# Optimization experiments

Hardware: AMD Instinct MI355X
Metric: run time of the kernel (lower is better)

## Reference

```python
import jax, jax.numpy as jnp
import numpy as np

NEG_MASK = -999.0  # matches masked_fill_(-999) in the torch source

def setup_inputs() -> dict:
    key = jax.random.key(0)
    ks = jax.random.split(key, 8)
    B, N, D = 4, 2048, 768      # batch, nodes, in_dim
    H, Do = 6, 128              # att_head, out_dim (D == H*Do)
    feat_in = jax.random.normal(ks[0], (B, N, D), dtype=jnp.float32)
    adj = jax.random.randint(ks[1], (B, N, N), 0, 2).astype(jnp.int32)
    W = jax.random.normal(ks[2], (H, D, Do), dtype=jnp.float32) * (1.0 / np.sqrt(D))
    b = jnp.zeros((Do,), dtype=jnp.float32)
    w_src = jax.random.normal(ks[3], (H, Do, 1), dtype=jnp.float32) * (1.0 / np.sqrt(Do))
    w_dst = jax.random.normal(ks[4], (H, Do, 1), dtype=jnp.float32) * (1.0 / np.sqrt(Do))
    H_w = jax.random.normal(ks[5], (D, D), dtype=jnp.float32) * (1.0 / np.sqrt(D))
    H_b = jnp.zeros((D,), dtype=jnp.float32)
    return {"feat_in": feat_in, "adj": adj, "W": W, "b": b,
            "w_src": w_src, "w_dst": w_dst, "H_w": H_w, "H_b": H_b}

def reference(feat_in, adj, W, b, w_src, w_dst, H_w, H_b):
    leaky_alpha = 0.2
    B, N, D = feat_in.shape
    Hh = W.shape[0]
    # per-head projection: [B, H, N, Do]
    h = jnp.einsum('bni,hio->bhno', feat_in, W)
    th = jnp.tanh(h)
    attn_src = jnp.einsum('bhno,hoz->bhnz', th, w_src)  # [B,H,N,1]
    attn_dst = jnp.einsum('bhno,hoz->bhnz', th, w_dst)  # [B,H,N,1]
    # additive scores: src_i + dst_j -> [B,H,N,N]
    attn = attn_src + jnp.swapaxes(attn_dst, -1, -2)
    attn = jnp.where(attn >= 0, attn, leaky_alpha * attn)
    mask = (adj == 0)[:, None, :, :]  # [B,1,N,N]
    attn = jnp.where(mask, NEG_MASK, attn)
    attn = jax.nn.softmax(attn, axis=-1)
    feat_out = jnp.einsum('bhnm,bhmo->bhno', attn, h) + b  # [B,H,N,Do]
    feat_out = jnp.swapaxes(feat_out, 1, 2).reshape(B, N, -1)  # [B,N,H*Do]
    feat_out = jax.nn.elu(feat_out)
    gate = jax.nn.sigmoid(feat_in @ H_w.T + H_b)
    out = gate * feat_out + (1.0 - gate) * feat_in
    return out
```

## Files before the change

### kernel.cpp

```cpp
#include <hip/hip_runtime.h>
#include <hip/hip_bf16.h>

#define B_ 4
#define N_ 2048
#define D_ 768
#define H_ 6
#define Do_ 128
#define M_ (B_*N_)
#define C2_ (2*D_)
#define SROW 49152

typedef __attribute__((ext_vector_type(8))) short bf16x8;
typedef __attribute__((ext_vector_type(4))) float f32x4;
typedef __attribute__((ext_vector_type(4))) int int4v;
typedef __attribute__((ext_vector_type(2))) int int2v;
typedef __attribute__((ext_vector_type(4))) float float4v;
typedef __attribute__((ext_vector_type(4))) unsigned short ushort4v;

__device__ __forceinline__ float b2f(short s){
    unsigned u = ((unsigned)(unsigned short)s) << 16;
    return __builtin_bit_cast(float, u);
}
__device__ __forceinline__ short f2b(float f){
    unsigned u = __builtin_bit_cast(unsigned, f);
    unsigned r = (u + 0x7fffu + ((u >> 16) & 1u)) >> 16;
    return (short)r;
}
__device__ __forceinline__ int pk2(float a, float b){
    unsigned ua = __builtin_bit_cast(unsigned, a) + 0x8000u;
    unsigned ub = __builtin_bit_cast(unsigned, b) + 0x8000u;
    return (int)__builtin_amdgcn_perm(ub, ua, 0x07060302u);
}
__device__ __forceinline__ float fast_tanh(float x){
    float a = fabsf(x);
    float e = __expf(-2.0f * a);
    float t = (1.0f - e) / (1.0f + e);
    return copysignf(t, x);
}

__global__ __launch_bounds__(256) void k_prep_pack(const float* __restrict__ W,
                                                   const float* __restrict__ Hw,
                                                   const int* __restrict__ adj,
                                                   short* __restrict__ bmat,
                                                   unsigned char* __restrict__ pk){
    int bid = blockIdx.x, t = threadIdx.x;
    if (bid < C2_){
        int c = bid;
        if (c < D_){
            int hd = c >> 7, o = c & 127;
            const float* wp = W + hd*D_*Do_ + o;
            for (int k = t; k < D_; k += 256) bmat[c*D_ + k] = f2b(wp[k*Do_]);
        } else {
            int d = c - D_;
            const float* hp = Hw + d*D_;
            for (int k = t; k < D_; k += 256) bmat[c*D_ + k] = f2b(hp[k]);
        }
    } else {
        int g = (bid - C2_)*256 + t;
        const int* ap = adj + (size_t)g*8;
        int4v a0 = *(const int4v*)ap;
        int4v a1 = *(const int4v*)(ap + 4);
        unsigned by = 0;
        #pragma unroll
        for (int i = 0; i < 4; i++){
            by |= (a0[i] ? 1u : 0u) << i;
            by |= (a1[i] ? 1u : 0u) << (i + 4);
        }
        pk[g] = (unsigned char)by;
    }
}

__global__ __launch_bounds__(256) void k_gemm(const float* __restrict__ A,
                                              const short* __restrict__ Bm,
                                              short* __restrict__ ht,
                                              float* outg){
    __shared__ short As[128][72];
    __shared__ short Bs[128][72];
    int tid = threadIdx.x;
    int mBase = blockIdx.y * 128, cBase = blockIdx.x * 128;
    int wave = tid >> 6, lane = tid & 63, q = lane >> 4, nL = lane & 15;
    int wr = (wave >> 1) * 64, wc = (wave & 1) * 64;
    f32x4 acc[4][4] = {};
    for (int kk = 0; kk < D_; kk += 64){
        __syncthreads();
        #pragma unroll
        for (int i = 0; i < 8; i++){
            int idx = tid + i*256;
            int row = idx >> 4, c4 = (idx & 15) * 4;
            float4v av = *(const float4v*)&A[(mBase+row)*D_ + kk + c4];
            int2v w; w[0] = pk2(av[0], av[1]); w[1] = pk2(av[2], av[3]);
            *(int2v*)&As[row][c4] = w;
        }
        #pragma unroll
        for (int i = 0; i < 4; i++){
            int idx = tid + i*256;
            int row = idx >> 3, cs = (idx & 7) * 8;
            *(int4v*)&Bs[row][cs] = *(const int4v*)&Bm[(cBase+row)*D_ + kk + cs];
        }
        __syncthreads();
        #pragma unroll
        for (int k2 = 0; k2 < 64; k2 += 32){
            bf16x8 aF[4], bF[4];
            #pragma unroll
            for (int rt = 0; rt < 4; rt++) aF[rt] = *(const bf16x8*)&As[wr + rt*16 + nL][k2 + q*8];
            #pragma unroll
            for (int ct = 0; ct < 4; ct++) bF[ct] = *(const bf16x8*)&Bs[wc + ct*16 + nL][k2 + q*8];
            #pragma unroll
            for (int rt = 0; rt < 4; rt++)
                #pragma unroll
                for (int ct = 0; ct < 4; ct++)
                    acc[rt][ct] = __builtin_amdgcn_mfma_f32_16x16x32_bf16(aF[rt], bF[ct], acc[rt][ct], 0, 0, 0);
        }
    }
    if (cBase < D_){
        int hd = cBase >> 7;
        #pragma unroll
        for (int rt = 0; rt < 4; rt++){
            #pragma unroll
            for (int ct = 0; ct < 4; ct++){
                int o  = (wc + ct*16 + nL) & 127;
                int m0 = mBase + wr + rt*16 + q*4;
                int b = m0 >> 11, n0 = m0 & 2047;
                ushort4v v;
                #pragma unroll
                for (int r = 0; r < 4; r++) v[r] = (unsigned short)f2b(acc[rt][ct][r]);
                *(ushort4v*)&ht[((b*H_ + hd)*Do_ + o)*N_ + n0] = v;
            }
        }
    } else {
        #pragma unroll
        for (int rt = 0; rt < 4; rt++){
            #pragma unroll
            for (int ct = 0; ct < 4; ct++){
                int d  = cBase - D_ + wc + ct*16 + nL;
                int m0 = mBase + wr + rt*16 + q*4;
                #pragma unroll
                for (int r = 0; r < 4; r++) outg[(size_t)(m0 + r)*D_ + d] = acc[rt][ct][r];
            }
        }
    }
}

__global__ __launch_bounds__(256) void k_stats(const short* __restrict__ ht,
                                               const float* __restrict__ wsrc,
                                               const float* __restrict__ wdst,
                                               float* __restrict__ srcP,
                                               float* __restrict__ dstP){
    int g = blockIdx.x * 256 + threadIdx.x;
    int y = blockIdx.y, o0 = y * 32;
    int bh = g >> 11, n = g & 2047;
    int hd = bh % H_;
    const short* hp = ht + bh*Do_*N_ + n + o0*N_;
    const float* ws = wsrc + hd*Do_ + o0;
    const float* wd = wdst + hd*Do_ + o0;
    float as = 0.f, ad = 0.f;
    for (int o = 0; o < 32; o++){
        float t = fast_tanh(b2f(hp[o*N_]));
        as += t * ws[o];
        ad += t * wd[o];
    }
    srcP[y*SROW + g] = as; dstP[y*SROW + g] = ad;
}

struct StageS {
    float E1[2048];
    float E2[2048];
    unsigned pkw[64*65];
};
struct RedS { float red[2][64][37]; };
union LdsU { StageS s; RedS r; };
__global__ __launch_bounds__(256) void k_pv(const unsigned char* __restrict__ pkG,
                                            const float* __restrict__ srcP,
                                            const float* __restrict__ dstP,
                                            const short* __restrict__ ht,
                                            const float* __restrict__ feat_in,
                                            const float* __restrict__ bias,
                                            const float* __restrict__ Hb,
                                            float* outg){
    __shared__ LdsU U;
    int itile = blockIdx.x, hd = blockIdx.y, b = blockIdx.z;
    int tid = threadIdx.x, wave = tid >> 6, lane = tid & 63, q = lane >> 4, nL = lane & 15;
    int rh = wave >> 1, kh = wave & 1;
    int r0 = itile * 64;
    int bh = b*H_ + hd;
    {
        const float4v* g0 = (const float4v*)(dstP + bh*N_);
        const float4v* g1 = (const float4v*)(dstP + SROW + bh*N_);
        const float4v* g2 = (const float4v*)(dstP + 2*SROW + bh*N_);
        const float4v* g3 = (const float4v*)(dstP + 3*SROW + bh*N_);
        #pragma unroll
        for (int h = 0; h < 2; h++){
            int c4 = tid*2 + h;
            float4v d = g0[c4] + g1[c4] + g2[c4] + g3[c4];
            #pragma unroll
            for (int t = 0; t < 4; t++){
                U.s.E1[c4*4 + t] = __expf(d[t]);
                U.s.E2[c4*4 + t] = __expf(0.2f * d[t]);
            }
        }
        const unsigned* pg = (const unsigned*)(pkG + (size_t)(b*N_ + r0) * (N_/8));
        #pragma unroll
        for (int k = 0; k < 16; k++){
            int idx = tid + k*256;
            U.s.pkw[(idx >> 6)*65 + (idx & 63)] = pg[idx];
        }
    }
    __syncthreads();
    int rowL0 = rh*32 + nL, rowL1 = rowL0 + 16;
    int gi0 = bh*N_ + r0 + rowL0, gi1 = bh*N_ + r0 + rowL1;
    float s0 = srcP[gi0] + srcP[SROW+gi0] + srcP[2*SROW+gi0] + srcP[3*SROW+gi0];
    float s1 = srcP[gi1] + srcP[SROW+gi1] + srcP[2*SROW+gi1] + srcP[3*SROW+gi1];
    float e1r0 = __expf(s0), e2r0 = __expf(0.2f*s0);
    float e1r1 = __expf(s1), e2r1 = __expf(0.2f*s1);
    bf16x8 vone;
    #pragma unroll
    for (int t = 0; t < 8; t++) vone[t] = (short)0x3F80;
    const short* hp = ht + bh*Do_*N_;
    f32x4 acc[2][8] = {};
    f32x4 accl0 = {}, accl1 = {};
    int base0 = rowL0*65, base1 = rowL1*65;
    int jEnd = kh*1024 + 1024;
    for (int j0 = kh*1024; j0 < jEnd; j0 += 32){
        unsigned by0 = (U.s.pkw[base0 + (j0 >> 5)] >> (q*8)) & 0xFF;
        unsigned by1 = (U.s.pkw[base1 + (j0 >> 5)] >> (q*8)) & 0xFF;
        int kb = j0 + q*8;
        float4v E1a = *(const float4v*)&U.s.E1[kb];
        float4v E1b = *(const float4v*)&U.s.E1[kb + 4];
        float4v E2a = *(const float4v*)&U.s.E2[kb];
        float4v E2b = *(const float4v*)&U.s.E2[kb + 4];
        float p0[8], p1[8];
        #pragma unroll
        for (int t = 0; t < 8; t++){
            float E1t = t < 4 ? E1a[t] : E1b[t-4];
            float E2t = t < 4 ? E2a[t] : E2b[t-4];
            float a0 = fmaxf(e1r0*E1t, e2r0*E2t);
            float a1 = fmaxf(e1r1*E1t, e2r1*E2t);
            p0[t] = ((by0 >> t) & 1u) ? a0 : 0.0f;
            p1[t] = ((by1 >> t) & 1u) ? a1 : 0.0f;
        }
        int4v pi0, pi1;
        #pragma unroll
        for (int tp = 0; tp < 4; tp++){
            pi0[tp] = pk2(p0[2*tp], p0[2*tp+1]);
            pi1[tp] = pk2(p1[2*tp], p1[2*tp+1]);
        }
        bf16x8 pf0 = __builtin_bit_cast(bf16x8, pi0);
        bf16x8 pf1 = __builtin_bit_cast(bf16x8, pi1);
        #pragma unroll
        for (int ct = 0; ct < 8; ct++){
            bf16x8 bF = *(const bf16x8*)&hp[(ct*16 + nL)*N_ + kb];
            acc[0][ct] = __builtin_amdgcn_mfma_f32_16x16x32_bf16(pf0, bF, acc[0][ct], 0, 0, 0);
            acc[1][ct] = __builtin_amdgcn_mfma_f32_16x16x32_bf16(pf1, bF, acc[1][ct], 0, 0, 0);
        }
        accl0 = __builtin_amdgcn_mfma_f32_16x16x32_bf16(pf0, vone, accl0, 0, 0, 0);
        accl1 = __builtin_amdgcn_mfma_f32_16x16x32_bf16(pf1, vone, accl1, 0, 0, 0);
    }
    __syncthreads();
    if (kh == 1){
        #pragma unroll
        for (int ct = 0; ct < 8; ct++)
            #pragma unroll
            for (int r = 0; r < 4; r++) U.r.red[rh][lane][ct*4 + r] = acc[0][ct][r];
        #pragma unroll
        for (int r = 0; r < 4; r++) U.r.red[rh][lane][32 + r] = accl0[r];
    }
    __syncthreads();
    if (kh == 0){
        #pragma unroll
        for (int ct = 0; ct < 8; ct++)
            #pragma unroll
            for (int r = 0; r < 4; r++) acc[0][ct][r] += U.r.red[rh][lane][ct*4 + r];
        #pragma unroll
        for (int r = 0; r < 4; r++) accl0[r] += U.r.red[rh][lane][32 + r];
    }
    __syncthreads();
    if (kh == 0){
        #pragma unroll
        for (int ct = 0; ct < 8; ct++)
            #pragma unroll
            for (int r = 0; r < 4; r++) U.r.red[rh][lane][ct*4 + r] = acc[1][ct][r];
        #pragma unroll
        for (int r = 0; r < 4; r++) U.r.red[rh][lane][32 + r] = accl1[r];
    }
    __syncthreads();
    if (kh == 1){
        #pragma unroll
        for (int ct = 0; ct < 8; ct++)
            #pragma unroll
            for (int r = 0; r < 4; r++) acc[1][ct][r] += U.r.red[rh][lane][ct*4 + r];
        #pragma unroll
        for (int r = 0; r < 4; r++) accl1[r] += U.r.red[rh][lane][32 + r];
    }
    {
        int f = kh;
        f32x4 accl = f ? accl1 : accl0;
        #pragma unroll
        for (int r = 0; r < 4; r++){
            int i = r0 + rh*32 + f*16 + q*4 + r;
            float invl = 1.0f / accl[r];
            size_t base = (size_t)(b*N_ + i)*D_ + hd*Do_;
            #pragma unroll
            for (int ct = 0; ct < 8; ct++){
                int o = ct*16 + nL;
                float v = acc[f][ct][r]*invl + bias[o];
                float e = v > 0.f ? v : __expf(v) - 1.0f;
                float gl = outg[base + o] + Hb[hd*Do_ + o];
                float g = 1.0f / (1.0f + __expf(-gl));
                float fi = feat_in[base + o];
                outg[base + o] = g*e + (1.0f - g)*fi;
            }
        }
    }
}

extern "C" void kernel_launch(void* const* d_in, const int* in_sizes, int n_in,
                              void* d_out, int out_size, void* d_ws, size_t ws_size,
                              hipStream_t stream){
    const float* feat = (const float*)d_in[0];
    const int*   adj  = (const int*)  d_in[1];
    const float* W    = (const float*)d_in[2];
    const float* bias = (const float*)d_in[3];
    const float* wsrc = (const float*)d_in[4];
    const float* wdst = (const float*)d_in[5];
    const float* Hw   = (const float*)d_in[6];
    const float* Hb   = (const float*)d_in[7];
    float* out = (float*)d_out;
    char* ws = (char*)d_ws;
    short* bmat = (short*)(ws);
    short* ht   = (short*)(ws + 2359296);
    float* srcP = (float*)(ws + 14942208);
    float* dstP = (float*)(ws + 15728640);
    unsigned char* pk = (unsigned char*)(ws + 16515072);

    hipLaunchKernelGGL(k_prep_pack, dim3(C2_ + 8192), dim3(256), 0, stream, W, Hw, adj, bmat, pk);
    hipLaunchKernelGGL(k_gemm,      dim3(12, 64),     dim3(256), 0, stream, feat, bmat, ht, out);
    hipLaunchKernelGGL(k_stats,     dim3(192, 4),     dim3(256), 0, stream, ht, wsrc, wdst, srcP, dstP);
    hipLaunchKernelGGL(k_pv,        dim3(32, 6, 4),   dim3(256), 0, stream, pk, srcP, dstP,
                       ht, feat, bias, Hb, out);
}
```

Before: 317.6 us.

## Tile ht layout, async global-to-LDS loads, swizzled LDS, XCD-aware block remap

Changes the projected-feature buffer to a tiled [bh][n/32][o][32] layout so the attention PV kernel reads contiguous 64-byte chunks instead of rows strided by N. The GEMM now loads fp32 A and bf16 B directly into XOR-swizzled LDS via global_load_lds, converts to bf16 with the hardware pack instruction at fragment-load time, and stages the gate-output epilogue through LDS for coalesced float4 stores. Both GEMM and PV grids are flattened and remapped so consecutive blocks spread across the 8 XCDs. The PV inner loop uses packed float2 math, bit-field-extract masks and v_cvt_pk_bf16_f32 in place of a select-then-pack sequence. In exchange the A tile stays fp32 in LDS, doubling its footprint, and the cvt happens repeatedly per wave.

```diff
diff --git a/kernel.cpp b/kernel.cpp
--- a/kernel.cpp
+++ b/kernel.cpp
@@ -13,8 +13,8 @@
 typedef __attribute__((ext_vector_type(8))) short bf16x8;
 typedef __attribute__((ext_vector_type(4))) float f32x4;
 typedef __attribute__((ext_vector_type(4))) int int4v;
-typedef __attribute__((ext_vector_type(2))) int int2v;
 typedef __attribute__((ext_vector_type(4))) float float4v;
+typedef __attribute__((ext_vector_type(2))) float float2v;
 typedef __attribute__((ext_vector_type(4))) unsigned short ushort4v;
 
 __device__ __forceinline__ float b2f(short s){
@@ -26,10 +26,10 @@
     unsigned r = (u + 0x7fffu + ((u >> 16) & 1u)) >> 16;
     return (short)r;
 }
-__device__ __forceinline__ int pk2(float a, float b){
-    unsigned ua = __builtin_bit_cast(unsigned, a) + 0x8000u;
-    unsigned ub = __builtin_bit_cast(unsigned, b) + 0x8000u;
-    return (int)__builtin_amdgcn_perm(ub, ua, 0x07060302u);
+__device__ __forceinline__ int cvtpk(float lo, float hi){
+    int r;
+    asm("v_cvt_pk_bf16_f32 %0, %1, %2" : "=v"(r) : "v"(lo), "v"(hi));
+    return r;
 }
 __device__ __forceinline__ float fast_tanh(float x){
     float a = fabsf(x);
@@ -37,6 +37,13 @@
     float t = (1.0f - e) / (1.0f + e);
     return copysignf(t, x);
 }
+__device__ __forceinline__ void gload_lds16(const void* g, void* l){
+    __builtin_amdgcn_global_load_lds((const __attribute__((address_space(1))) unsigned int*)g,
+                                     (__attribute__((address_space(3))) unsigned int*)l,
+                                     16, 0, 0);
+}
+
+#define HT_IDX(bh, n, o) ((((size_t)((bh)*64 + ((n) >> 5))*128 + (o))*32) + ((n) & 31))
 
 __global__ __launch_bounds__(256) void k_prep_pack(const float* __restrict__ W,
                                                    const float* __restrict__ Hw,
@@ -70,41 +77,59 @@
     }
 }
 
-__global__ __launch_bounds__(256) void k_gemm(const float* __restrict__ A,
+union GS {
+    struct { float A[8192]; short B[8192]; } s;
+    float t[12288];
+};
+__global__ __launch_bounds__(256) void k_gemm(const float* __restrict__ Af,
                                               const short* __restrict__ Bm,
                                               short* __restrict__ ht,
                                               float* outg){
-    __shared__ short As[128][72];
-    __shared__ short Bs[128][72];
-    int tid = threadIdx.x;
-    int mBase = blockIdx.y * 128, cBase = blockIdx.x * 128;
-    int wave = tid >> 6, lane = tid & 63, q = lane >> 4, nL = lane & 15;
+    __shared__ GS G;
+    int lid = blockIdx.x;
+    int nid = (lid & 7)*96 + (lid >> 3);
+    int bx = nid % 12, by = nid / 12;
+    int mBase = by * 128, cBase = bx * 128;
+    int tid = threadIdx.x, wave = tid >> 6, lane = tid & 63, q = lane >> 4, nL = lane & 15;
     int wr = (wave >> 1) * 64, wc = (wave & 1) * 64;
+    int arow = tid >> 4;
+    int alu  = (tid & 15) ^ (arow & 7);
+    const float* aSrc = Af + (size_t)(mBase + arow)*D_ + alu*4;
+    float* aDst = G.t + wave*256;
+    int brow = tid >> 3;
+    int blu  = (tid & 7) ^ (brow & 7);
+    const short* bSrc = Bm + (size_t)(cBase + brow)*D_ + blu*8;
+    short* bDst = G.s.B + wave*512;
     f32x4 acc[4][4] = {};
     for (int kk = 0; kk < D_; kk += 64){
         __syncthreads();
         #pragma unroll
-        for (int i = 0; i < 8; i++){
-            int idx = tid + i*256;
-            int row = idx >> 4, c4 = (idx & 15) * 4;
-            float4v av = *(const float4v*)&A[(mBase+row)*D_ + kk + c4];
-            int2v w; w[0] = pk2(av[0], av[1]); w[1] = pk2(av[2], av[3]);
-            *(int2v*)&As[row][c4] = w;
-        }
-        #pragma unroll
-        for (int i = 0; i < 4; i++){
-            int idx = tid + i*256;
-            int row = idx >> 3, cs = (idx & 7) * 8;
-            *(int4v*)&Bs[row][cs] = *(const int4v*)&Bm[(cBase+row)*D_ + kk + cs];
-        }
+        for (int i = 0; i < 8; i++)
+            gload_lds16(aSrc + (size_t)i*16*D_ + kk, aDst + i*1024);
+        #pragma unroll
+        for (int i = 0; i < 4; i++)
+            gload_lds16(bSrc + (size_t)i*32*D_ + kk, bDst + i*2048);
         __syncthreads();
         #pragma unroll
         for (int k2 = 0; k2 < 64; k2 += 32){
+            int ub = (k2 >> 2) + q*2;
             bf16x8 aF[4], bF[4];
             #pragma unroll
-            for (int rt = 0; rt < 4; rt++) aF[rt] = *(const bf16x8*)&As[wr + rt*16 + nL][k2 + q*8];
-            #pragma unroll
-            for (int ct = 0; ct < 4; ct++) bF[ct] = *(const bf16x8*)&Bs[wc + ct*16 + nL][k2 + q*8];
+            for (int rt = 0; rt < 4; rt++){
+                int r = wr + rt*16 + nL;
+                const float* Ar = &G.s.A[r*64];
+                float4v x0 = *(const float4v*)&Ar[(ub ^ (r & 7)) << 2];
+                float4v x1 = *(const float4v*)&Ar[((ub+1) ^ (r & 7)) << 2];
+                int4v w = { cvtpk(x0[0], x0[1]), cvtpk(x0[2], x0[3]),
+                            cvtpk(x1[0], x1[1]), cvtpk(x1[2], x1[3]) };
+                aF[rt] = __builtin_bit_cast(bf16x8, w);
+            }
+            int cb = (k2 >> 3) + q;
+            #pragma unroll
+            for (int ct = 0; ct < 4; ct++){
+                int r = wc + ct*16 + nL;
+                bF[ct] = *(const bf16x8*)&G.s.B[r*64 + ((cb ^ (r & 7)) * 8)];
+            }
             #pragma unroll
             for (int rt = 0; rt < 4; rt++)
                 #pragma unroll
@@ -121,22 +146,33 @@
                 int o  = (wc + ct*16 + nL) & 127;
                 int m0 = mBase + wr + rt*16 + q*4;
                 int b = m0 >> 11, n0 = m0 & 2047;
+                int bh = b*H_ + hd;
                 ushort4v v;
                 #pragma unroll
                 for (int r = 0; r < 4; r++) v[r] = (unsigned short)f2b(acc[rt][ct][r]);
-                *(ushort4v*)&ht[((b*H_ + hd)*Do_ + o)*N_ + n0] = v;
+                *(ushort4v*)&ht[HT_IDX(bh, n0, o)] = v;
             }
         }
     } else {
+        __syncthreads();
+        int dQ = cBase - D_ + wc;
+        float* Ts = G.t + wave*1088;
+        int row = lane >> 2, cbs = (lane & 3) * 16;
         #pragma unroll
         for (int rt = 0; rt < 4; rt++){
             #pragma unroll
-            for (int ct = 0; ct < 4; ct++){
-                int d  = cBase - D_ + wc + ct*16 + nL;
-                int m0 = mBase + wr + rt*16 + q*4;
+            for (int ct = 0; ct < 4; ct++)
                 #pragma unroll
-                for (int r = 0; r < 4; r++) outg[(size_t)(m0 + r)*D_ + d] = acc[rt][ct][r];
-            }
+                for (int r = 0; r < 4; r++)
+                    Ts[(q*4 + r)*68 + ct*16 + nL] = acc[rt][ct][r];
+            __builtin_amdgcn_sched_barrier(0);
+            int gm = mBase + wr + rt*16 + row;
+            #pragma unroll
+            for (int c4 = 0; c4 < 4; c4++){
+                float4v v = *(const float4v*)&Ts[row*68 + cbs + c4*4];
+                *(float4v*)&outg[(size_t)gm*D_ + dQ + cbs + c4*4] = v;
+            }
+            __builtin_amdgcn_sched_barrier(0);
         }
     }
 }
@@ -150,12 +186,12 @@
     int y = blockIdx.y, o0 = y * 32;
     int bh = g >> 11, n = g & 2047;
     int hd = bh % H_;
-    const short* hp = ht + bh*Do_*N_ + n + o0*N_;
+    const short* hp = ht + HT_IDX(bh, n, o0);
     const float* ws = wsrc + hd*Do_ + o0;
     const float* wd = wdst + hd*Do_ + o0;
     float as = 0.f, ad = 0.f;
     for (int o = 0; o < 32; o++){
-        float t = fast_tanh(b2f(hp[o*N_]));
+        float t = fast_tanh(b2f(hp[o*32]));
         as += t * ws[o];
         ad += t * wd[o];
     }
@@ -178,7 +214,10 @@
                                             const float* __restrict__ Hb,
                                             float* outg){
     __shared__ LdsU U;
-    int itile = blockIdx.x, hd = blockIdx.y, b = blockIdx.z;
+    int lid = blockIdx.x;
+    int nid = (lid & 7)*96 + (lid >> 3);
+    int itile = nid & 31;
+    int hd = (nid >> 5) % 6, b = nid / 192;
     int tid = threadIdx.x, wave = tid >> 6, lane = tid & 63, q = lane >> 4, nL = lane & 15;
     int rh = wave >> 1, kh = wave & 1;
     int r0 = itile * 64;
@@ -210,12 +249,12 @@
     int gi0 = bh*N_ + r0 + rowL0, gi1 = bh*N_ + r0 + rowL1;
     float s0 = srcP[gi0] + srcP[SROW+gi0] + srcP[2*SROW+gi0] + srcP[3*SROW+gi0];
     float s1 = srcP[gi1] + srcP[SROW+gi1] + srcP[2*SROW+gi1] + srcP[3*SROW+gi1];
-    float e1r0 = __expf(s0), e2r0 = __expf(0.2f*s0);
-    float e1r1 = __expf(s1), e2r1 = __expf(0.2f*s1);
+    float2v e1v0 = {__expf(s0), __expf(s0)}, e2v0 = {__expf(0.2f*s0), __expf(0.2f*s0)};
+    float2v e1v1 = {__expf(s1), __expf(s1)}, e2v1 = {__expf(0.2f*s1), __expf(0.2f*s1)};
     bf16x8 vone;
     #pragma unroll
     for (int t = 0; t < 8; t++) vone[t] = (short)0x3F80;
-    const short* hp = ht + bh*Do_*N_;
+    const short* hp = ht + (size_t)bh*262144;
     f32x4 acc[2][8] = {};
     f32x4 accl0 = {}, accl1 = {};
     int base0 = rowL0*65, base1 = rowL1*65;
@@ -224,31 +263,29 @@
         unsigned by0 = (U.s.pkw[base0 + (j0 >> 5)] >> (q*8)) & 0xFF;
         unsigned by1 = (U.s.pkw[base1 + (j0 >> 5)] >> (q*8)) & 0xFF;
         int kb = j0 + q*8;
-        float4v E1a = *(const float4v*)&U.s.E1[kb];
-        float4v E1b = *(const float4v*)&U.s.E1[kb + 4];
-        float4v E2a = *(const float4v*)&U.s.E2[kb];
-        float4v E2b = *(const float4v*)&U.s.E2[kb + 4];
-        float p0[8], p1[8];
-        #pragma unroll
-        for (int t = 0; t < 8; t++){
-            float E1t = t < 4 ? E1a[t] : E1b[t-4];
-            float E2t = t < 4 ? E2a[t] : E2b[t-4];
-            float a0 = fmaxf(e1r0*E1t, e2r0*E2t);
-            float a1 = fmaxf(e1r1*E1t, e2r1*E2t);
-            p0[t] = ((by0 >> t) & 1u) ? a0 : 0.0f;
-            p1[t] = ((by1 >> t) & 1u) ? a1 : 0.0f;
-        }
-        int4v pi0, pi1;
+        const short* hj = hp + (size_t)(j0 >> 5)*4096 + q*8;
+        const float2v* E1p = (const float2v*)&U.s.E1[kb];
+        const float2v* E2p = (const float2v*)&U.s.E2[kb];
+        int w0[4], w1[4];
         #pragma unroll
         for (int tp = 0; tp < 4; tp++){
-            pi0[tp] = pk2(p0[2*tp], p0[2*tp+1]);
-            pi1[tp] = pk2(p1[2*tp], p1[2*tp+1]);
-        }
+            float2v E1t = E1p[tp], E2t = E2p[tp];
+            float2v a0 = __builtin_elementwise_max(e1v0*E1t, e2v0*E2t);
+            float2v a1 = __builtin_elementwise_max(e1v1*E1t, e2v1*E2t);
+            int m00 = __builtin_amdgcn_sbfe((int)by0, 2*tp,   1);
+            int m01 = __builtin_amdgcn_sbfe((int)by0, 2*tp+1, 1);
+            int m10 = __builtin_amdgcn_sbfe((int)by1, 2*tp,   1);
+            int m11 = __builtin_amdgcn_sbfe((int)by1, 2*tp+1, 1);
+            w0[tp] = cvtpk(a0[0], a0[1]) & (int)__builtin_amdgcn_perm((unsigned)m01, (unsigned)m00, 0x05040100u);
+            w1[tp] = cvtpk(a1[0], a1[1]) & (int)__builtin_amdgcn_perm((unsigned)m11, (unsigned)m10, 0x05040100u);
+        }
+        int4v pi0 = {w0[0], w0[1], w0[2], w0[3]};
+        int4v pi1 = {w1[0], w1[1], w1[2], w1[3]};
         bf16x8 pf0 = __builtin_bit_cast(bf16x8, pi0);
         bf16x8 pf1 = __builtin_bit_cast(bf16x8, pi1);
         #pragma unroll
         for (int ct = 0; ct < 8; ct++){
-            bf16x8 bF = *(const bf16x8*)&hp[(ct*16 + nL)*N_ + kb];
+            bf16x8 bF = *(const bf16x8*)&hj[(ct*16 + nL)*32];
             acc[0][ct] = __builtin_amdgcn_mfma_f32_16x16x32_bf16(pf0, bF, acc[0][ct], 0, 0, 0);
             acc[1][ct] = __builtin_amdgcn_mfma_f32_16x16x32_bf16(pf1, bF, acc[1][ct], 0, 0, 0);
         }
@@ -333,8 +370,8 @@
     unsigned char* pk = (unsigned char*)(ws + 16515072);
 
     hipLaunchKernelGGL(k_prep_pack, dim3(C2_ + 8192), dim3(256), 0, stream, W, Hw, adj, bmat, pk);
-    hipLaunchKernelGGL(k_gemm,      dim3(12, 64),     dim3(256), 0, stream, feat, bmat, ht, out);
+    hipLaunchKernelGGL(k_gemm,      dim3(768),        dim3(256), 0, stream, feat, bmat, ht, out);
     hipLaunchKernelGGL(k_stats,     dim3(192, 4),     dim3(256), 0, stream, ht, wsrc, wdst, srcP, dstP);
-    hipLaunchKernelGGL(k_pv,        dim3(32, 6, 4),   dim3(256), 0, stream, pk, srcP, dstP,
+    hipLaunchKernelGGL(k_pv,        dim3(768),        dim3(256), 0, stream, pk, srcP, dstP,
                        ht, feat, bias, Hb, out);
 }
```

New measurement: 287.1 us. 1.11x faster.

## Tile ht layout, remap grids for XCD locality, widen k_pv to 512 threads

Applied to the files above, without the earlier changes.

Changes the projected-feature buffer to a tiled layout (32-node chunks × 128 features), so the P·V B-fragment loads in k_pv and the strided loads in k_stats read contiguous 64-byte chunks instead of rows 4 KB apart. Remaps the GEMM and attention grids to 1D with an XCD-aware swizzle so blocks sharing data land on the same XCD and its L2. Stages the gate-GEMM output through LDS so it is written to global memory as coalesced float4 stores. k_pv now runs 8 waves, each handling 16 rows instead of 32, which raises parallelism but doubles the ht fragment loads per row tile and changes occupancy.

```diff
diff --git a/kernel.cpp b/kernel.cpp
--- a/kernel.cpp
+++ b/kernel.cpp
@@ -37,6 +37,8 @@
     float t = (1.0f - e) / (1.0f + e);
     return copysignf(t, x);
 }
+
+#define HT_IDX(bh, n, o) ((((size_t)((bh)*64 + ((n) >> 5))*128 + (o))*32) + ((n) & 31))
 
 __global__ __launch_bounds__(256) void k_prep_pack(const float* __restrict__ W,
                                                    const float* __restrict__ Hw,
@@ -76,8 +78,11 @@
                                               float* outg){
     __shared__ short As[128][72];
     __shared__ short Bs[128][72];
+    int lid = blockIdx.x;
+    int xcd = lid & 7, s = lid >> 3;
+    int bx = s >> 3, by = xcd*8 + (s & 7);
     int tid = threadIdx.x;
-    int mBase = blockIdx.y * 128, cBase = blockIdx.x * 128;
+    int mBase = by * 128, cBase = bx * 128;
     int wave = tid >> 6, lane = tid & 63, q = lane >> 4, nL = lane & 15;
     int wr = (wave >> 1) * 64, wc = (wave & 1) * 64;
     f32x4 acc[4][4] = {};
@@ -121,22 +126,33 @@
                 int o  = (wc + ct*16 + nL) & 127;
                 int m0 = mBase + wr + rt*16 + q*4;
                 int b = m0 >> 11, n0 = m0 & 2047;
+                int bh = b*H_ + hd;
                 ushort4v v;
                 #pragma unroll
                 for (int r = 0; r < 4; r++) v[r] = (unsigned short)f2b(acc[rt][ct][r]);
-                *(ushort4v*)&ht[((b*H_ + hd)*Do_ + o)*N_ + n0] = v;
+                *(ushort4v*)&ht[HT_IDX(bh, n0, o)] = v;
             }
         }
     } else {
+        __syncthreads();
+        int dQ = cBase - D_ + wc;
+        float* Ts = (float*)As + wave*1088;
+        int row = lane >> 2, cbs = (lane & 3) * 16;
         #pragma unroll
         for (int rt = 0; rt < 4; rt++){
             #pragma unroll
-            for (int ct = 0; ct < 4; ct++){
-                int d  = cBase - D_ + wc + ct*16 + nL;
-                int m0 = mBase + wr + rt*16 + q*4;
+            for (int ct = 0; ct < 4; ct++)
                 #pragma unroll
-                for (int r = 0; r < 4; r++) outg[(size_t)(m0 + r)*D_ + d] = acc[rt][ct][r];
+                for (int r = 0; r < 4; r++)
+                    Ts[(q*4 + r)*68 + ct*16 + nL] = acc[rt][ct][r];
+            __builtin_amdgcn_sched_barrier(0);
+            int gm = mBase + wr + rt*16 + row;
+            #pragma unroll
+            for (int c4 = 0; c4 < 4; c4++){
+                float4v v = *(const float4v*)&Ts[row*68 + cbs + c4*4];
+                *(float4v*)&outg[(size_t)gm*D_ + dQ + cbs + c4*4] = v;
             }
+            __builtin_amdgcn_sched_barrier(0);
         }
     }
 }
@@ -150,12 +166,12 @@
     int y = blockIdx.y, o0 = y * 32;
     int bh = g >> 11, n = g & 2047;
     int hd = bh % H_;
-    const short* hp = ht + bh*Do_*N_ + n + o0*N_;
+    const short* hp = ht + HT_IDX(bh, n, o0);
     const float* ws = wsrc + hd*Do_ + o0;
     const float* wd = wdst + hd*Do_ + o0;
     float as = 0.f, ad = 0.f;
     for (int o = 0; o < 32; o++){
-        float t = fast_tanh(b2f(hp[o*N_]));
+        float t = fast_tanh(b2f(hp[o*32]));
         as += t * ws[o];
         ad += t * wd[o];
     }
@@ -167,9 +183,9 @@
     float E2[2048];
     unsigned pkw[64*65];
 };
-struct RedS { float red[2][64][37]; };
+struct RedS { float red[4][64][37]; };
 union LdsU { StageS s; RedS r; };
-__global__ __launch_bounds__(256) void k_pv(const unsigned char* __restrict__ pkG,
+__global__ __launch_bounds__(512) void k_pv(const unsigned char* __restrict__ pkG,
                                             const float* __restrict__ srcP,
                                             const float* __restrict__ dstP,
                                             const short* __restrict__ ht,
@@ -178,7 +194,10 @@
                                             const float* __restrict__ Hb,
                                             float* outg){
     __shared__ LdsU U;
-    int itile = blockIdx.x, hd = blockIdx.y, b = blockIdx.z;
+    int lid = blockIdx.x;
+    int nid = (lid & 7)*96 + (lid >> 3);
+    int itile = nid & 31;
+    int hd = (nid >> 5) % 6, b = nid / 192;
     int tid = threadIdx.x, wave = tid >> 6, lane = tid & 63, q = lane >> 4, nL = lane & 15;
     int rh = wave >> 1, kh = wave & 1;
     int r0 = itile * 64;
@@ -188,126 +207,91 @@
         const float4v* g1 = (const float4v*)(dstP + SROW + bh*N_);
         const float4v* g2 = (const float4v*)(dstP + 2*SROW + bh*N_);
         const float4v* g3 = (const float4v*)(dstP + 3*SROW + bh*N_);
-        #pragma unroll
-        for (int h = 0; h < 2; h++){
-            int c4 = tid*2 + h;
-            float4v d = g0[c4] + g1[c4] + g2[c4] + g3[c4];
-            #pragma unroll
-            for (int t = 0; t < 4; t++){
-                U.s.E1[c4*4 + t] = __expf(d[t]);
-                U.s.E2[c4*4 + t] = __expf(0.2f * d[t]);
-            }
+        int c4 = tid;
+        float4v d = g0[c4] + g1[c4] + g2[c4] + g3[c4];
+        #pragma unroll
+        for (int t = 0; t < 4; t++){
+            U.s.E1[c4*4 + t] = __expf(d[t]);
+            U.s.E2[c4*4 + t] = __expf(0.2f * d[t]);
         }
         const unsigned* pg = (const unsigned*)(pkG + (size_t)(b*N_ + r0) * (N_/8));
         #pragma unroll
-        for (int k = 0; k < 16; k++){
-            int idx = tid + k*256;
+        for (int k = 0; k < 8; k++){
+            int idx = tid + k*512;
             U.s.pkw[(idx >> 6)*65 + (idx & 63)] = pg[idx];
         }
     }
     __syncthreads();
-    int rowL0 = rh*32 + nL, rowL1 = rowL0 + 16;
-    int gi0 = bh*N_ + r0 + rowL0, gi1 = bh*N_ + r0 + rowL1;
-    float s0 = srcP[gi0] + srcP[SROW+gi0] + srcP[2*SROW+gi0] + srcP[3*SROW+gi0];
-    float s1 = srcP[gi1] + srcP[SROW+gi1] + srcP[2*SROW+gi1] + srcP[3*SROW+gi1];
-    float e1r0 = __expf(s0), e2r0 = __expf(0.2f*s0);
-    float e1r1 = __expf(s1), e2r1 = __expf(0.2f*s1);
+    int rowL = rh*16 + nL;
+    int gi = bh*N_ + r0 + rowL;
+    float sv = srcP[gi] + srcP[SROW+gi] + srcP[2*SROW+gi] + srcP[3*SROW+gi];
+    float e1r = __expf(sv), e2r = __expf(0.2f*sv);
     bf16x8 vone;
     #pragma unroll
     for (int t = 0; t < 8; t++) vone[t] = (short)0x3F80;
-    const short* hp = ht + bh*Do_*N_;
-    f32x4 acc[2][8] = {};
-    f32x4 accl0 = {}, accl1 = {};
-    int base0 = rowL0*65, base1 = rowL1*65;
+    const short* hp = ht + (size_t)bh*262144;
+    f32x4 acc[8] = {};
+    f32x4 accl = {};
+    int base = rowL*65;
     int jEnd = kh*1024 + 1024;
     for (int j0 = kh*1024; j0 < jEnd; j0 += 32){
-        unsigned by0 = (U.s.pkw[base0 + (j0 >> 5)] >> (q*8)) & 0xFF;
-        unsigned by1 = (U.s.pkw[base1 + (j0 >> 5)] >> (q*8)) & 0xFF;
+        unsigned by = (U.s.pkw[base + (j0 >> 5)] >> (q*8)) & 0xFF;
         int kb = j0 + q*8;
+        const short* hj = hp + (size_t)(j0 >> 5)*4096 + q*8;
         float4v E1a = *(const float4v*)&U.s.E1[kb];
         float4v E1b = *(const float4v*)&U.s.E1[kb + 4];
         float4v E2a = *(const float4v*)&U.s.E2[kb];
         float4v E2b = *(const float4v*)&U.s.E2[kb + 4];
-        float p0[8], p1[8];
+        float p[8];
         #pragma unroll
         for (int t = 0; t < 8; t++){
             float E1t = t < 4 ? E1a[t] : E1b[t-4];
             float E2t = t < 4 ? E2a[t] : E2b[t-4];
-            float a0 = fmaxf(e1r0*E1t, e2r0*E2t);
-            float a1 = fmaxf(e1r1*E1t, e2r1*E2t);
-            p0[t] = ((by0 >> t) & 1u) ? a0 : 0.0f;
-            p1[t] = ((by1 >> t) & 1u) ? a1 : 0.0f;
-        }
-        int4v pi0, pi1;
-        #pragma unroll
-        for (int tp = 0; tp < 4; tp++){
-            pi0[tp] = pk2(p0[2*tp], p0[2*tp+1]);
-            pi1[tp] = pk2(p1[2*tp], p1[2*tp+1]);
-        }
-        bf16x8 pf0 = __builtin_bit_cast(bf16x8, pi0);
-        bf16x8 pf1 = __builtin_bit_cast(bf16x8, pi1);
+            float a = fmaxf(e1r*E1t, e2r*E2t);
+            p[t] = ((by >> t) & 1u) ? a : 0.0f;
+        }
+        int4v pi;
+        #pragma unroll
+        for (int tp = 0; tp < 4; tp++) pi[tp] = pk2(p[2*tp], p[2*tp+1]);
+        bf16x8 pf = __builtin_bit_cast(bf16x8, pi);
         #pragma unroll
         for (int ct = 0; ct < 8; ct++){
-            bf16x8 bF = *(const bf16x8*)&hp[(ct*16 + nL)*N_ + kb];
-            acc[0][ct] = __builtin_amdgcn_mfma_f32_16x16x32_bf16(pf0, bF, acc[0][ct], 0, 0, 0);
-            acc[1][ct] = __builtin_amdgcn_mfma_f32_16x16x32_bf16(pf1, bF, acc[1][ct], 0, 0, 0);
-        }
-        accl0 = __builtin_amdgcn_mfma_f32_16x16x32_bf16(pf0, vone, accl0, 0, 0, 0);
-        accl1 = __builtin_amdgcn_mfma_f32_16x16x32_bf16(pf1, vone, accl1, 0, 0, 0);
+            bf16x8 bF = *(const bf16x8*)&hj[(ct*16 + nL)*32];
+            acc[ct] = __builtin_amdgcn_mfma_f32_16x16x32_bf16(pf, bF, acc[ct], 0, 0, 0);
+        }
+        accl = __builtin_amdgcn_mfma_f32_16x16x32_bf16(pf, vone, accl, 0, 0, 0);
     }
     __syncthreads();
     if (kh == 1){
         #pragma unroll
         for (int ct = 0; ct < 8; ct++)
             #pragma unroll
-            for (int r = 0; r < 4; r++) U.r.red[rh][lane][ct*4 + r] = acc[0][ct][r];
-        #pragma unroll
-        for (int r = 0; r < 4; r++) U.r.red[rh][lane][32 + r] = accl0[r];
+            for (int r = 0; r < 4; r++) U.r.red[rh][lane][ct*4 + r] = acc[ct][r];
+        #pragma unroll
+        for (int r = 0; r < 4; r++) U.r.red[rh][lane][32 + r] = accl[r];
     }
     __syncthreads();
     if (kh == 0){
         #pragma unroll
         for (int ct = 0; ct < 8; ct++)
             #pragma unroll
-            for (int r = 0; r < 4; r++) acc[0][ct][r] += U.r.red[rh][lane][ct*4 + r];
-        #pragma unroll
-        for (int r = 0; r < 4; r++) accl0[r] += U.r.red[rh][lane][32 + r];
-    }
-    __syncthreads();
-    if (kh == 0){
-        #pragma unroll
-        for (int ct = 0; ct < 8; ct++)
-            #pragma unroll
-            for (int r = 0; r < 4; r++) U.r.red[rh][lane][ct*4 + r] = acc[1][ct][r];
-        #pragma unroll
-        for (int r = 0; r < 4; r++) U.r.red[rh][lane][32 + r] = accl1[r];
-    }
-    __syncthreads();
-    if (kh == 1){
-        #pragma unroll
-        for (int ct = 0; ct < 8; ct++)
-            #pragma unroll
-            for (int r = 0; r < 4; r++) acc[1][ct][r] += U.r.red[rh][lane][ct*4 + r];
-        #pragma unroll
-        for (int r = 0; r < 4; r++) accl1[r] += U.r.red[rh][lane][32 + r];
-    }
-    {
-        int f = kh;
-        f32x4 accl = f ? accl1 : accl0;
+            for (int r = 0; r < 4; r++) acc[ct][r] += U.r.red[rh][lane][ct*4 + r];
+        #pragma unroll
+        for (int r = 0; r < 4; r++) accl[r] += U.r.red[rh][lane][32 + r];
         #pragma unroll
         for (int r = 0; r < 4; r++){
-            int i = r0 + rh*32 + f*16 + q*4 + r;
+            int i = r0 + rh*16 + q*4 + r;
             float invl = 1.0f / accl[r];
-            size_t base = (size_t)(b*N_ + i)*D_ + hd*Do_;
+            size_t baseO = (size_t)(b*N_ + i)*D_ + hd*Do_;
             #pragma unroll
             for (int ct = 0; ct < 8; ct++){
                 int o = ct*16 + nL;
-                float v = acc[f][ct][r]*invl + bias[o];
+                float v = acc[ct][r]*invl + bias[o];
                 float e = v > 0.f ? v : __expf(v) - 1.0f;
-                float gl = outg[base + o] + Hb[hd*Do_ + o];
+                float gl = outg[baseO + o] + Hb[hd*Do_ + o];
                 float g = 1.0f / (1.0f + __expf(-gl));
-                float fi = feat_in[base + o];
-                outg[base + o] = g*e + (1.0f - g)*fi;
+                float fi = feat_in[baseO + o];
+                outg[baseO + o] = g*e + (1.0f - g)*fi;
             }
         }
     }
@@ -333,8 +317,8 @@
     unsigned char* pk = (unsigned char*)(ws + 16515072);
 
     hipLaunchKernelGGL(k_prep_pack, dim3(C2_ + 8192), dim3(256), 0, stream, W, Hw, adj, bmat, pk);
-    hipLaunchKernelGGL(k_gemm,      dim3(12, 64),     dim3(256), 0, stream, feat, bmat, ht, out);
+    hipLaunchKernelGGL(k_gemm,      dim3(768),        dim3(256), 0, stream, feat, bmat, ht, out);
     hipLaunchKernelGGL(k_stats,     dim3(192, 4),     dim3(256), 0, stream, ht, wsrc, wdst, srcP, dstP);
-    hipLaunchKernelGGL(k_pv,        dim3(32, 6, 4),   dim3(256), 0, stream, pk, srcP, dstP,
+    hipLaunchKernelGGL(k_pv,        dim3(768),        dim3(512), 0, stream, pk, srcP, dstP,
                        ht, feat, bias, Hb, out);
 }
```

Result: faster. 300.8 us (-5.3%).
